# Kernel tuning notes

Measured on AMD Instinct MI355X. Metric: run time of the kernel, lower is better.

The kernel has to match this reference:

```python
import jax, jax.numpy as jnp
import numpy as np

B, N, D, H, DK, DV = 2, 2048, 1024, 16, 64, 64
NEG = -1000000000.0
EPS = 1e-6


def setup_inputs() -> dict:
    key = jax.random.key(0)
    ks = jax.random.split(key, 8)
    s = 0.02
    return {
        "q": jax.random.normal(ks[0], (B, N, D), jnp.float32),
        "k": jax.random.normal(ks[1], (B, N, D), jnp.float32),
        "v": jax.random.normal(ks[2], (B, N, D), jnp.float32),
        "attn_mask": jnp.ones((B, N, N), jnp.int32),
        "Wq": jax.random.normal(ks[3], (D, H * DK), jnp.float32) * s,
        "Wk": jax.random.normal(ks[4], (D, H * DK), jnp.float32) * s,
        "Wv": jax.random.normal(ks[5], (D, H * DV), jnp.float32) * s,
        "Wo": jax.random.normal(ks[6], (H * DV, D), jnp.float32) * s,
        "gamma": jnp.ones((D,), jnp.float32),
        "beta": jnp.zeros((D,), jnp.float32),
    }


def reference(q, k, v, attn_mask, Wq, Wk, Wv, Wo, gamma, beta):
    b, n, _ = q.shape
    residual = q
    # project and split heads: (b, h, n, dk)
    qh = (q @ Wq).reshape(b, n, H, DK).transpose(0, 2, 1, 3)
    kh = (k @ Wk).reshape(b, n, H, DK).transpose(0, 2, 1, 3)
    vh = (v @ Wv).reshape(b, n, H, DV).transpose(0, 2, 1, 3)
    temperature = DK ** 0.5
    scores = jnp.einsum('bhnd,bhmd->bhnm', qh / temperature, kh)
    # external mask (masked where mask == 0), broadcast over heads
    scores = jnp.where(attn_mask[:, None, :, :] == 0, NEG, scores)
    # built-in causal mask (strictly upper triangle)
    causal = jnp.triu(jnp.ones((n, n), dtype=bool), k=1)
    scores = jnp.where(causal, NEG, scores)
    attn = jax.nn.softmax(scores, axis=-1)
    out = jnp.einsum('bhnm,bhmd->bnhd', attn, vh).reshape(b, n, H * DV)
    out = out @ Wo + residual
    # LayerNorm(eps=1e-6)
    mean = out.mean(-1, keepdims=True)
    var = ((out - mean) ** 2).mean(-1, keepdims=True)
    out = (out - mean) / jnp.sqrt(var + EPS) * gamma + beta
    return out, attn
```

## Files before the change

### kernel.cpp

```cpp
#include <hip/hip_runtime.h>
#include <hip/hip_bf16.h>
#include <stdint.h>

#define B_ 2
#define N_ 2048
#define D_ 1024
#define H_ 16
#define MM 4096
#define NN 1024
#define KK 1024

typedef __bf16 bf16;
typedef __bf16 bf16x8 __attribute__((ext_vector_type(8)));
typedef float f32x4 __attribute__((ext_vector_type(4)));

struct __align__(8) bf4 { bf16 v[4]; };

#define LDS_STRIDE 144

#define GLDS(gp, lp)                                                     \
    __builtin_amdgcn_global_load_lds(                                    \
        (const __attribute__((address_space(1))) void*)(gp),             \
        (__attribute__((address_space(3))) void*)(lp), 16, 0, 0)

__global__ __launch_bounds__(256) void k_cvt3(const float* __restrict__ q,
                                              const float* __restrict__ k,
                                              const float* __restrict__ v,
                                              bf16* __restrict__ qb,
                                              bf16* __restrict__ kb,
                                              bf16* __restrict__ vb) {
    const int z = blockIdx.y;
    const float* s = z == 0 ? q : z == 1 ? k : v;
    bf16* d = z == 0 ? qb : z == 1 ? kb : vb;
    size_t i = ((size_t)blockIdx.x * 256 + threadIdx.x) * 8;
    f32x4 a = *(const f32x4*)(s + i);
    f32x4 b = *(const f32x4*)(s + i + 4);
    bf16x8 o;
#pragma unroll
    for (int j = 0; j < 4; ++j) { o[j] = (bf16)a[j]; o[4 + j] = (bf16)b[j]; }
    *(bf16x8*)(d + i) = o;
}

__global__ void k_wtt(const float* __restrict__ W, bf16* __restrict__ Wt) {
    __shared__ float t[32][33];
    int bx = blockIdx.x * 32, by = blockIdx.y * 32;
    int tx = threadIdx.x, ty = threadIdx.y;
#pragma unroll
    for (int j = 0; j < 32; j += 8)
        t[ty + j][tx] = W[(size_t)(by + ty + j) * 1024 + bx + tx];
    __syncthreads();
#pragma unroll
    for (int j = 0; j < 32; j += 8)
        Wt[(size_t)(bx + ty + j) * 1024 + by + tx] = (bf16)t[tx][ty + j];
}

__global__ __launch_bounds__(256) void k_bits(const int* __restrict__ mask,
                                              uint32_t* __restrict__ bits) {
    size_t flat = (size_t)blockIdx.x * 256 + threadIdx.x;
    int col = (int)(flat & (N_ - 1));
    int row = (int)((flat >> 11) & (N_ - 1));
    bool ok = (mask[flat] != 0) && (col <= row);
    unsigned long long bal = __ballot(ok);
    if ((threadIdx.x & 63) == 0)
        *(unsigned long long*)(bits + (flat >> 5)) = bal;
}

__device__ __forceinline__ void mm_core(const bf16* __restrict__ A,
                                        const bf16* __restrict__ Bt,
                                        int bm0, int bn0,
                                        bf16* As, bf16* Bs,
                                        f32x4 (&acc)[4][4]) {
    const int tid = threadIdx.x, w = tid >> 6, lane = tid & 63;
    const int g = lane >> 4, li = lane & 15;
    const int wr = w >> 1, wc = w & 1;
    const int row = tid >> 3, cc = tid & 7;

    f32x4 zz = {0.f, 0.f, 0.f, 0.f};
#pragma unroll
    for (int mf = 0; mf < 4; ++mf)
#pragma unroll
        for (int nf = 0; nf < 4; ++nf) acc[mf][nf] = zz;

    auto stage = [&](int k0) {
#pragma unroll
        for (int c = 0; c < 4; ++c) {
            int ch = c * 256 + tid;
            int r = ch >> 3, cl = ch & 7;
            GLDS(A + (size_t)(bm0 + r) * KK + k0 + cl * 8,
                 As + ((size_t)c * 256 + w * 64) * 8);
        }
#pragma unroll
        for (int c = 0; c < 4; ++c) {
            int ch = c * 256 + tid;
            int r = ch >> 3, cl = ch & 7;
            GLDS(Bt + (size_t)(bn0 + r) * KK + k0 + cl * 8,
                 Bs + ((size_t)c * 256 + w * 64) * 8);
        }
    };
    (void)row; (void)cc;

    stage(0);
    for (int s = 0; s < KK / 64; ++s) {
        __syncthreads();
#pragma unroll
        for (int kk = 0; kk < 2; ++kk) {
            bf16x8 af[4], bfr[4];
#pragma unroll
            for (int i = 0; i < 4; ++i) {
                af[i] = *(const bf16x8*)(As + (wr * 64 + i * 16 + li) * 64 + kk * 32 + g * 8);
                bfr[i] = *(const bf16x8*)(Bs + (wc * 64 + i * 16 + li) * 64 + kk * 32 + g * 8);
            }
#pragma unroll
            for (int mf = 0; mf < 4; ++mf)
#pragma unroll
                for (int nf = 0; nf < 4; ++nf)
                    acc[mf][nf] = __builtin_amdgcn_mfma_f32_16x16x32_bf16(
                        af[mf], bfr[nf], acc[mf][nf], 0, 0, 0);
        }
        __syncthreads();
        if (s + 1 < KK / 64) stage((s + 1) * 64);
    }
}

__global__ __launch_bounds__(256) void k_proj(const bf16* __restrict__ qb,
                                              const bf16* __restrict__ kb,
                                              const bf16* __restrict__ vb,
                                              const bf16* __restrict__ WqT,
                                              const bf16* __restrict__ WkT,
                                              const bf16* __restrict__ WvT,
                                              bf16* __restrict__ Qh,
                                              bf16* __restrict__ Kh,
                                              bf16* __restrict__ Vt) {
    __shared__ __align__(16) bf16 As[128 * 64];
    __shared__ __align__(16) bf16 Bs[128 * 64];
    const int z = blockIdx.y;
    const bf16* A = z == 0 ? qb : z == 1 ? kb : vb;
    const bf16* Bt = z == 0 ? WqT : z == 1 ? WkT : WvT;
    int bid = blockIdx.x;
    int swz = (bid & 7) * 32 + (bid >> 3);
    int bm0 = (swz >> 3) * 128, bn0 = (swz & 7) * 128;

    f32x4 acc[4][4];
    mm_core(A, Bt, bm0, bn0, As, Bs, acc);

    const int tid = threadIdx.x, w = tid >> 6, lane = tid & 63;
    const int g = lane >> 4, li = lane & 15;
    const int wr = w >> 1, wc = w & 1;
    const float scale = (z == 0) ? 0.125f : 1.0f;

    if (z < 2) {
        bf16* C = (z == 0) ? Qh : Kh;
#pragma unroll
        for (int mf = 0; mf < 4; ++mf)
#pragma unroll
            for (int nf = 0; nf < 4; ++nf) {
                int m0 = bm0 + wr * 64 + mf * 16 + g * 4;
                int n = bn0 + wc * 64 + nf * 16 + li;
#pragma unroll
                for (int r = 0; r < 4; ++r)
                    C[(size_t)(m0 + r) * NN + n] = (bf16)(acc[mf][nf][r] * scale);
            }
    } else {
#pragma unroll
        for (int mf = 0; mf < 4; ++mf)
#pragma unroll
            for (int nf = 0; nf < 4; ++nf) {
                int m0 = bm0 + wr * 64 + mf * 16 + g * 4;
                int n = bn0 + wc * 64 + nf * 16 + li;
                int bq = m0 >> 11, tok = m0 & (N_ - 1);
                int hh = n >> 6, dv = n & 63;
                bf4 val;
#pragma unroll
                for (int r = 0; r < 4; ++r) val.v[r] = (bf16)acc[mf][nf][r];
                *(bf4*)(Vt + ((size_t)((bq * H_ + hh) * 64 + dv)) * N_ + tok) = val;
            }
    }
}

__global__ __launch_bounds__(256) void k_out(const bf16* __restrict__ Ob,
                                             const bf16* __restrict__ WoT,
                                             float* __restrict__ outp,
                                             const float* __restrict__ resid) {
    __shared__ __align__(16) bf16 As[128 * 64];
    __shared__ __align__(16) bf16 Bs[128 * 64];
    int bid = blockIdx.x;
    int swz = (bid & 7) * 32 + (bid >> 3);
    int bm0 = (swz >> 3) * 128, bn0 = (swz & 7) * 128;

    f32x4 acc[4][4];
    mm_core(Ob, WoT, bm0, bn0, As, Bs, acc);

    const int tid = threadIdx.x, w = tid >> 6, lane = tid & 63;
    const int g = lane >> 4, li = lane & 15;
    const int wr = w >> 1, wc = w & 1;
#pragma unroll
    for (int mf = 0; mf < 4; ++mf)
#pragma unroll
        for (int nf = 0; nf < 4; ++nf) {
            int m0 = bm0 + wr * 64 + mf * 16 + g * 4;
            int n = bn0 + wc * 64 + nf * 16 + li;
#pragma unroll
            for (int r = 0; r < 4; ++r) {
                size_t ix = (size_t)(m0 + r) * NN + n;
                outp[ix] = acc[mf][nf][r] + resid[ix];
            }
        }
}

__global__ __launch_bounds__(256) void k_attn(const bf16* __restrict__ Qh,
                                              const bf16* __restrict__ Kh,
                                              const bf16* __restrict__ Vt,
                                              const uint32_t* __restrict__ bits,
                                              float* __restrict__ attnp,
                                              bf16* __restrict__ Ob) {
    __shared__ __align__(16) char Qs[64 * LDS_STRIDE];
    __shared__ __align__(16) char Ks[2][64 * LDS_STRIDE];
    __shared__ __align__(16) char Vs[2][64 * LDS_STRIDE];
    __shared__ __align__(16) char Ps[64 * LDS_STRIDE];
    const int tid = threadIdx.x, lane = tid & 63, w = tid >> 6;
    const int g = lane >> 4, li = lane & 15;
    const int p = blockIdx.x, h = blockIdx.y, b = blockIdx.z;
    const int srow = tid >> 3, sc = tid & 7;
    const int myrow = w * 16 + li;

    const size_t kbase = ((size_t)b * N_) * D_ + h * 64;
    const size_t vbase = ((size_t)(b * H_ + h) * 64) * N_;
    f32x4 zz = {0.f, 0.f, 0.f, 0.f};

    bf16x8 ka, kb2, va, vb2;
    auto loadK = [&](int jt) {
        const char* ks = (const char*)Kh +
            (kbase + (size_t)(jt * 64 + srow) * D_ + sc * 8) * 2;
        ka = *(const bf16x8*)ks;
        kb2 = *(const bf16x8*)(ks + (size_t)32 * D_ * 2);
    };
    auto loadV = [&](int jt) {
        const char* vs = (const char*)Vt +
            (vbase + (size_t)srow * N_ + jt * 64 + sc * 8) * 2;
        va = *(const bf16x8*)vs;
        vb2 = *(const bf16x8*)(vs + (size_t)32 * N_ * 2);
    };
    auto writeK = [&](int bi) {
        *(bf16x8*)(Ks[bi] + srow * LDS_STRIDE + sc * 16) = ka;
        *(bf16x8*)(Ks[bi] + (srow + 32) * LDS_STRIDE + sc * 16) = kb2;
    };
    auto writeV = [&](int bi) {
        *(bf16x8*)(Vs[bi] + srow * LDS_STRIDE + sc * 16) = va;
        *(bf16x8*)(Vs[bi] + (srow + 32) * LDS_STRIDE + sc * 16) = vb2;
    };

    for (int half = 0; half < 2; ++half) {
        const int qt = half ? (31 - p) : p;
        const int i0 = qt << 6;
        const size_t abase = (((size_t)b * H_ + h) * N_ + i0) * (size_t)N_;

        __syncthreads();
        {
            const char* qsrc = (const char*)Qh +
                (kbase + (size_t)(i0 + srow) * D_ + sc * 8) * 2;
            bf16x8 t0 = *(const bf16x8*)qsrc;
            bf16x8 t1 = *(const bf16x8*)(qsrc + (size_t)32 * D_ * 2);
            *(bf16x8*)(Qs + srow * LDS_STRIDE + sc * 16) = t0;
            *(bf16x8*)(Qs + (srow + 32) * LDS_STRIDE + sc * 16) = t1;
        }
        const uint32_t* mrow = bits + (((size_t)b * N_ + i0 + myrow) << 6);

        float m = -1e30f, l = 0.f;
        loadK(0);
        writeK(0);
        for (int jt = 0; jt <= qt; ++jt) {
            if (jt < qt) loadK(jt + 1);
            uint2 mw = *(const uint2*)(mrow + (jt << 1));
            __syncthreads();
            const char* Kb = Ks[jt & 1];

            f32x4 s[4];
#pragma unroll
            for (int mf = 0; mf < 4; ++mf) s[mf] = zz;
#pragma unroll
            for (int kk = 0; kk < 2; ++kk) {
                const int kb = kk * 64 + (g << 4);
                bf16x8 qf = *(const bf16x8*)(Qs + myrow * LDS_STRIDE + kb);
#pragma unroll
                for (int mf = 0; mf < 4; ++mf) {
                    bf16x8 kf = *(const bf16x8*)(Kb + (mf * 16 + li) * LDS_STRIDE + kb);
                    s[mf] = __builtin_amdgcn_mfma_f32_16x16x32_bf16(kf, qf, s[mf], 0, 0, 0);
                }
            }
            if (jt < qt) writeK((jt + 1) & 1);

            float tmax = m;
#pragma unroll
            for (int mf = 0; mf < 4; ++mf) {
                uint32_t wsel = (mf < 2) ? mw.x : mw.y;
#pragma unroll
                for (int r = 0; r < 4; ++r) {
                    int sh = (mf & 1) * 16 + g * 4 + r;
                    float xv = ((wsel >> sh) & 1) ? s[mf][r] : -1e9f;
                    s[mf][r] = xv;
                    tmax = fmaxf(tmax, xv);
                }
            }
            tmax = fmaxf(tmax, __shfl_xor(tmax, 16));
            tmax = fmaxf(tmax, __shfl_xor(tmax, 32));
            float ps = 0.f;
#pragma unroll
            for (int mf = 0; mf < 4; ++mf)
#pragma unroll
                for (int r = 0; r < 4; ++r) ps += __expf(s[mf][r] - tmax);
            ps += __shfl_xor(ps, 16);
            ps += __shfl_xor(ps, 32);
            l = l * __expf(m - tmax) + ps;
            m = tmax;
        }
        const float linv = 1.0f / l;

        f32x4 oacc[4];
#pragma unroll
        for (int nf = 0; nf < 4; ++nf) oacc[nf] = zz;

        __syncthreads();
        loadK(0);
        loadV(0);
        writeK(0);
        writeV(0);
        for (int jt = 0; jt <= qt; ++jt) {
            if (jt < qt) { loadK(jt + 1); loadV(jt + 1); }
            uint2 mw = *(const uint2*)(mrow + (jt << 1));
            __syncthreads();
            const char* Kb = Ks[jt & 1];
            const char* Vb = Vs[jt & 1];

            f32x4 s[4];
#pragma unroll
            for (int mf = 0; mf < 4; ++mf) s[mf] = zz;
#pragma unroll
            for (int kk = 0; kk < 2; ++kk) {
                const int kb = kk * 64 + (g << 4);
                bf16x8 qf = *(const bf16x8*)(Qs + myrow * LDS_STRIDE + kb);
#pragma unroll
                for (int mf = 0; mf < 4; ++mf) {
                    bf16x8 kf = *(const bf16x8*)(Kb + (mf * 16 + li) * LDS_STRIDE + kb);
                    s[mf] = __builtin_amdgcn_mfma_f32_16x16x32_bf16(kf, qf, s[mf], 0, 0, 0);
                }
            }
            if (jt < qt) { writeK((jt + 1) & 1); writeV((jt + 1) & 1); }

#pragma unroll
            for (int mf = 0; mf < 4; ++mf) {
                uint32_t wsel = (mf < 2) ? mw.x : mw.y;
#pragma unroll
                for (int r = 0; r < 4; ++r) {
                    int sh = (mf & 1) * 16 + g * 4 + r;
                    float xv = ((wsel >> sh) & 1) ? s[mf][r] : -1e9f;
                    s[mf][r] = __expf(xv - m) * linv;
                }
                __builtin_nontemporal_store(s[mf],
                    (f32x4*)(attnp + abase + (size_t)myrow * N_ + (jt << 6) + mf * 16 + g * 4));
                bf4 pk;
#pragma unroll
                for (int r = 0; r < 4; ++r) pk.v[r] = (bf16)s[mf][r];
                *(bf4*)(Ps + myrow * LDS_STRIDE + (mf * 16 + g * 4) * 2) = pk;
            }
#pragma unroll
            for (int kk = 0; kk < 2; ++kk) {
                const int kb = kk * 64 + (g << 4);
                bf16x8 pf = *(const bf16x8*)(Ps + myrow * LDS_STRIDE + kb);
#pragma unroll
                for (int nf = 0; nf < 4; ++nf) {
                    bf16x8 vf = *(const bf16x8*)(Vb + (nf * 16 + li) * LDS_STRIDE + kb);
                    oacc[nf] = __builtin_amdgcn_mfma_f32_16x16x32_bf16(pf, vf, oacc[nf], 0, 0, 0);
                }
            }
        }
#pragma unroll
        for (int nf = 0; nf < 4; ++nf)
#pragma unroll
            for (int r = 0; r < 4; ++r) {
                int gi = i0 + w * 16 + g * 4 + r;
                Ob[((size_t)(b * N_ + gi)) * D_ + h * 64 + nf * 16 + li] = (bf16)oacc[nf][r];
            }
        int zc0 = i0 + 64;
        if (zc0 < N_) {
            int r = tid >> 2, tc = tid & 3;
            f32x4 z = zz;
            for (int c = zc0 + tc * 4; c < N_; c += 16)
                __builtin_nontemporal_store(z, (f32x4*)(attnp + abase + (size_t)r * N_ + c));
        }
    }
}

__global__ __launch_bounds__(256) void k_ln(float* __restrict__ out,
                                            const float* __restrict__ gamma,
                                            const float* __restrict__ beta) {
    const int row = blockIdx.x, t = threadIdx.x, lane = t & 63, w = t >> 6;
    float* p = out + (size_t)row * D_;
    f32x4 x = *(const f32x4*)(p + t * 4);
    float s = x[0] + x[1] + x[2] + x[3];
    float s2 = x[0] * x[0] + x[1] * x[1] + x[2] * x[2] + x[3] * x[3];
#pragma unroll
    for (int o = 1; o < 64; o <<= 1) {
        s += __shfl_xor(s, o);
        s2 += __shfl_xor(s2, o);
    }
    __shared__ float r1[4], r2[4];
    if (lane == 0) { r1[w] = s; r2[w] = s2; }
    __syncthreads();
    s = r1[0] + r1[1] + r1[2] + r1[3];
    s2 = r2[0] + r2[1] + r2[2] + r2[3];
    float mean = s * (1.f / D_);
    float var = s2 * (1.f / D_) - mean * mean;
    float rstd = rsqrtf(var + 1e-6f);
    f32x4 gv = *(const f32x4*)(gamma + t * 4);
    f32x4 bv = *(const f32x4*)(beta + t * 4);
    f32x4 y;
#pragma unroll
    for (int c = 0; c < 4; ++c) y[c] = (x[c] - mean) * rstd * gv[c] + bv[c];
    *(f32x4*)(p + t * 4) = y;
}

extern "C" void kernel_launch(void* const* d_in, const int* in_sizes, int n_in,
                              void* d_out, int out_size, void* d_ws,
                              size_t ws_size, hipStream_t stream) {
    (void)in_sizes; (void)n_in; (void)out_size; (void)ws_size;
    const float* q = (const float*)d_in[0];
    const float* k = (const float*)d_in[1];
    const float* v = (const float*)d_in[2];
    const int* msk = (const int*)d_in[3];
    const float* Wq = (const float*)d_in[4];
    const float* Wk = (const float*)d_in[5];
    const float* Wv = (const float*)d_in[6];
    const float* Wo = (const float*)d_in[7];
    const float* gamma = (const float*)d_in[8];
    const float* beta = (const float*)d_in[9];

    float* outp = (float*)d_out;
    float* attnp = outp + (size_t)B_ * N_ * D_;

    const size_t U = (size_t)B_ * N_ * D_;
    const size_t W1 = (size_t)D_ * D_;
    bf16* ws = (bf16*)d_ws;
    bf16* qb = ws;   ws += U;
    bf16* kb = ws;   ws += U;
    bf16* vb = ws;   ws += U;
    bf16* WqT = ws;  ws += W1;
    bf16* WkT = ws;  ws += W1;
    bf16* WvT = ws;  ws += W1;
    bf16* WoT = ws;  ws += W1;
    bf16* Qh = ws;   ws += U;
    bf16* Kh = ws;   ws += U;
    bf16* Vt = ws;   ws += U;
    bf16* Ob = ws;   ws += U;
    uint32_t* bits = (uint32_t*)ws;

    k_cvt3<<<dim3(U / 8 / 256, 3), 256, 0, stream>>>(q, k, v, qb, kb, vb);
    dim3 tb(32, 8);
    k_wtt<<<dim3(32, 32), tb, 0, stream>>>(Wq, WqT);
    k_wtt<<<dim3(32, 32), tb, 0, stream>>>(Wk, WkT);
    k_wtt<<<dim3(32, 32), tb, 0, stream>>>(Wv, WvT);
    k_wtt<<<dim3(32, 32), tb, 0, stream>>>(Wo, WoT);
    k_bits<<<(size_t)B_ * N_ * N_ / 256, 256, 0, stream>>>(msk, bits);

    k_proj<<<dim3(256, 3), 256, 0, stream>>>(qb, kb, vb, WqT, WkT, WvT, Qh, Kh, Vt);

    k_attn<<<dim3(16, H_, B_), 256, 0, stream>>>(Qh, Kh, Vt, bits, attnp, Ob);

    k_out<<<256, 256, 0, stream>>>(Ob, WoT, outp, q);

    k_ln<<<B_ * N_, 256, 0, stream>>>(outp, gamma, beta);
}
```

Baseline: 300.2 us.

## Restructure attention into single-wave 16-row blocks with direct global K/V loads

Rewrites the attention kernel so each 64-thread block handles a 16-row query strip, paired with its mirrored strip for causal load balance. K and V fragments are read straight from global memory into registers instead of being staged through double-buffered LDS behind barriers. Blocks are mapped to (batch, head) so blocks sharing K/V land on the same XCD, for L2 reuse. The four weight-transpose launches are merged into one, trading launch overhead and more repeated global K/V reads for finer parallelism and no syncthreads.

```diff
diff --git a/kernel.cpp b/kernel.cpp
--- a/kernel.cpp
+++ b/kernel.cpp
@@ -41,7 +41,13 @@
     *(bf16x8*)(d + i) = o;
 }
 
-__global__ void k_wtt(const float* __restrict__ W, bf16* __restrict__ Wt) {
+__global__ void k_wtt4(const float* __restrict__ Wq, const float* __restrict__ Wk,
+                       const float* __restrict__ Wv, const float* __restrict__ Wo,
+                       bf16* __restrict__ WqT, bf16* __restrict__ WkT,
+                       bf16* __restrict__ WvT, bf16* __restrict__ WoT) {
+    const int z = blockIdx.z;
+    const float* W = z == 0 ? Wq : z == 1 ? Wk : z == 2 ? Wv : Wo;
+    bf16* Wt = z == 0 ? WqT : z == 1 ? WkT : z == 2 ? WvT : WoT;
     __shared__ float t[32][33];
     int bx = blockIdx.x * 32, by = blockIdx.y * 32;
     int tx = threadIdx.x, ty = threadIdx.y;
@@ -73,7 +79,6 @@
     const int tid = threadIdx.x, w = tid >> 6, lane = tid & 63;
     const int g = lane >> 4, li = lane & 15;
     const int wr = w >> 1, wc = w & 1;
-    const int row = tid >> 3, cc = tid & 7;
 
     f32x4 zz = {0.f, 0.f, 0.f, 0.f};
 #pragma unroll
@@ -97,7 +102,6 @@
                  Bs + ((size_t)c * 256 + w * 64) * 8);
         }
     };
-    (void)row; (void)cc;
 
     stage(0);
     for (int s = 0; s < KK / 64; ++s) {
@@ -207,88 +211,48 @@
         }
 }
 
-__global__ __launch_bounds__(256) void k_attn(const bf16* __restrict__ Qh,
-                                              const bf16* __restrict__ Kh,
-                                              const bf16* __restrict__ Vt,
-                                              const uint32_t* __restrict__ bits,
-                                              float* __restrict__ attnp,
-                                              bf16* __restrict__ Ob) {
-    __shared__ __align__(16) char Qs[64 * LDS_STRIDE];
-    __shared__ __align__(16) char Ks[2][64 * LDS_STRIDE];
-    __shared__ __align__(16) char Vs[2][64 * LDS_STRIDE];
-    __shared__ __align__(16) char Ps[64 * LDS_STRIDE];
-    const int tid = threadIdx.x, lane = tid & 63, w = tid >> 6;
+__global__ __launch_bounds__(64) void k_attn(const bf16* __restrict__ Qh,
+                                             const bf16* __restrict__ Kh,
+                                             const bf16* __restrict__ Vt,
+                                             const uint32_t* __restrict__ bits,
+                                             float* __restrict__ attnp,
+                                             bf16* __restrict__ Ob) {
+    __shared__ __align__(16) char Ps[16 * LDS_STRIDE];
+    const int lane = threadIdx.x;
     const int g = lane >> 4, li = lane & 15;
-    const int p = blockIdx.x, h = blockIdx.y, b = blockIdx.z;
-    const int srow = tid >> 3, sc = tid & 7;
-    const int myrow = w * 16 + li;
-
-    const size_t kbase = ((size_t)b * N_) * D_ + h * 64;
+    const int id = blockIdx.x;
+    const int xcd = id & 7, slot = id >> 3;
+    const int c = xcd + 8 * (slot & 3);
+    const int p = slot >> 2;
+    const int h = c >> 1, b = c & 1;
+
+    const size_t cbase = ((size_t)b * N_) * D_ + h * 64;
     const size_t vbase = ((size_t)(b * H_ + h) * 64) * N_;
-    f32x4 zz = {0.f, 0.f, 0.f, 0.f};
-
-    bf16x8 ka, kb2, va, vb2;
-    auto loadK = [&](int jt) {
-        const char* ks = (const char*)Kh +
-            (kbase + (size_t)(jt * 64 + srow) * D_ + sc * 8) * 2;
-        ka = *(const bf16x8*)ks;
-        kb2 = *(const bf16x8*)(ks + (size_t)32 * D_ * 2);
-    };
-    auto loadV = [&](int jt) {
-        const char* vs = (const char*)Vt +
-            (vbase + (size_t)srow * N_ + jt * 64 + sc * 8) * 2;
-        va = *(const bf16x8*)vs;
-        vb2 = *(const bf16x8*)(vs + (size_t)32 * N_ * 2);
-    };
-    auto writeK = [&](int bi) {
-        *(bf16x8*)(Ks[bi] + srow * LDS_STRIDE + sc * 16) = ka;
-        *(bf16x8*)(Ks[bi] + (srow + 32) * LDS_STRIDE + sc * 16) = kb2;
-    };
-    auto writeV = [&](int bi) {
-        *(bf16x8*)(Vs[bi] + srow * LDS_STRIDE + sc * 16) = va;
-        *(bf16x8*)(Vs[bi] + (srow + 32) * LDS_STRIDE + sc * 16) = vb2;
-    };
+    const f32x4 zz = {0.f, 0.f, 0.f, 0.f};
 
     for (int half = 0; half < 2; ++half) {
-        const int qt = half ? (31 - p) : p;
-        const int i0 = qt << 6;
-        const size_t abase = (((size_t)b * H_ + h) * N_ + i0) * (size_t)N_;
-
-        __syncthreads();
-        {
-            const char* qsrc = (const char*)Qh +
-                (kbase + (size_t)(i0 + srow) * D_ + sc * 8) * 2;
-            bf16x8 t0 = *(const bf16x8*)qsrc;
-            bf16x8 t1 = *(const bf16x8*)(qsrc + (size_t)32 * D_ * 2);
-            *(bf16x8*)(Qs + srow * LDS_STRIDE + sc * 16) = t0;
-            *(bf16x8*)(Qs + (srow + 32) * LDS_STRIDE + sc * 16) = t1;
-        }
-        const uint32_t* mrow = bits + (((size_t)b * N_ + i0 + myrow) << 6);
+        const int sl = half ? (127 - p) : p;
+        const int qs0 = sl << 4;
+        const int jt_max = sl >> 2;
+        const size_t abase = (((size_t)b * H_ + h) * N_ + qs0) * (size_t)N_;
+
+        const bf16* qptr = Qh + cbase + (size_t)(qs0 + li) * D_ + g * 8;
+        const bf16x8 qf0 = *(const bf16x8*)qptr;
+        const bf16x8 qf1 = *(const bf16x8*)(qptr + 32);
+        const uint32_t* mrow = bits + (((size_t)b * N_ + qs0 + li) << 6);
 
         float m = -1e30f, l = 0.f;
-        loadK(0);
-        writeK(0);
-        for (int jt = 0; jt <= qt; ++jt) {
-            if (jt < qt) loadK(jt + 1);
-            uint2 mw = *(const uint2*)(mrow + (jt << 1));
-            __syncthreads();
-            const char* Kb = Ks[jt & 1];
-
+        for (int jt = 0; jt <= jt_max; ++jt) {
+            const uint2 mw = *(const uint2*)(mrow + (jt << 1));
+            const bf16* kptr = Kh + cbase + (size_t)(jt * 64 + li) * D_ + g * 8;
             f32x4 s[4];
 #pragma unroll
-            for (int mf = 0; mf < 4; ++mf) s[mf] = zz;
-#pragma unroll
-            for (int kk = 0; kk < 2; ++kk) {
-                const int kb = kk * 64 + (g << 4);
-                bf16x8 qf = *(const bf16x8*)(Qs + myrow * LDS_STRIDE + kb);
-#pragma unroll
-                for (int mf = 0; mf < 4; ++mf) {
-                    bf16x8 kf = *(const bf16x8*)(Kb + (mf * 16 + li) * LDS_STRIDE + kb);
-                    s[mf] = __builtin_amdgcn_mfma_f32_16x16x32_bf16(kf, qf, s[mf], 0, 0, 0);
-                }
-            }
-            if (jt < qt) writeK((jt + 1) & 1);
-
+            for (int mf = 0; mf < 4; ++mf) {
+                bf16x8 k0 = *(const bf16x8*)(kptr + (size_t)(mf * 16) * D_);
+                bf16x8 k1 = *(const bf16x8*)(kptr + (size_t)(mf * 16) * D_ + 32);
+                s[mf] = __builtin_amdgcn_mfma_f32_16x16x32_bf16(k0, qf0, zz, 0, 0, 0);
+                s[mf] = __builtin_amdgcn_mfma_f32_16x16x32_bf16(k1, qf1, s[mf], 0, 0, 0);
+            }
             float tmax = m;
 #pragma unroll
             for (int mf = 0; mf < 4; ++mf) {
@@ -319,33 +283,17 @@
 #pragma unroll
         for (int nf = 0; nf < 4; ++nf) oacc[nf] = zz;
 
-        __syncthreads();
-        loadK(0);
-        loadV(0);
-        writeK(0);
-        writeV(0);
-        for (int jt = 0; jt <= qt; ++jt) {
-            if (jt < qt) { loadK(jt + 1); loadV(jt + 1); }
-            uint2 mw = *(const uint2*)(mrow + (jt << 1));
-            __syncthreads();
-            const char* Kb = Ks[jt & 1];
-            const char* Vb = Vs[jt & 1];
-
+        for (int jt = 0; jt <= jt_max; ++jt) {
+            const uint2 mw = *(const uint2*)(mrow + (jt << 1));
+            const bf16* kptr = Kh + cbase + (size_t)(jt * 64 + li) * D_ + g * 8;
             f32x4 s[4];
 #pragma unroll
-            for (int mf = 0; mf < 4; ++mf) s[mf] = zz;
-#pragma unroll
-            for (int kk = 0; kk < 2; ++kk) {
-                const int kb = kk * 64 + (g << 4);
-                bf16x8 qf = *(const bf16x8*)(Qs + myrow * LDS_STRIDE + kb);
-#pragma unroll
-                for (int mf = 0; mf < 4; ++mf) {
-                    bf16x8 kf = *(const bf16x8*)(Kb + (mf * 16 + li) * LDS_STRIDE + kb);
-                    s[mf] = __builtin_amdgcn_mfma_f32_16x16x32_bf16(kf, qf, s[mf], 0, 0, 0);
-                }
-            }
-            if (jt < qt) { writeK((jt + 1) & 1); writeV((jt + 1) & 1); }
-
+            for (int mf = 0; mf < 4; ++mf) {
+                bf16x8 k0 = *(const bf16x8*)(kptr + (size_t)(mf * 16) * D_);
+                bf16x8 k1 = *(const bf16x8*)(kptr + (size_t)(mf * 16) * D_ + 32);
+                s[mf] = __builtin_amdgcn_mfma_f32_16x16x32_bf16(k0, qf0, zz, 0, 0, 0);
+                s[mf] = __builtin_amdgcn_mfma_f32_16x16x32_bf16(k1, qf1, s[mf], 0, 0, 0);
+            }
 #pragma unroll
             for (int mf = 0; mf < 4; ++mf) {
                 uint32_t wsel = (mf < 2) ? mw.x : mw.y;
@@ -356,37 +304,34 @@
                     s[mf][r] = __expf(xv - m) * linv;
                 }
                 __builtin_nontemporal_store(s[mf],
-                    (f32x4*)(attnp + abase + (size_t)myrow * N_ + (jt << 6) + mf * 16 + g * 4));
+                    (f32x4*)(attnp + abase + (size_t)li * N_ + (jt << 6) + mf * 16 + g * 4));
                 bf4 pk;
 #pragma unroll
                 for (int r = 0; r < 4; ++r) pk.v[r] = (bf16)s[mf][r];
-                *(bf4*)(Ps + myrow * LDS_STRIDE + (mf * 16 + g * 4) * 2) = pk;
-            }
-#pragma unroll
-            for (int kk = 0; kk < 2; ++kk) {
-                const int kb = kk * 64 + (g << 4);
-                bf16x8 pf = *(const bf16x8*)(Ps + myrow * LDS_STRIDE + kb);
-#pragma unroll
-                for (int nf = 0; nf < 4; ++nf) {
-                    bf16x8 vf = *(const bf16x8*)(Vb + (nf * 16 + li) * LDS_STRIDE + kb);
-                    oacc[nf] = __builtin_amdgcn_mfma_f32_16x16x32_bf16(pf, vf, oacc[nf], 0, 0, 0);
-                }
+                *(bf4*)(Ps + li * LDS_STRIDE + (mf * 16 + g * 4) * 2) = pk;
+            }
+            bf16x8 pf0 = *(const bf16x8*)(Ps + li * LDS_STRIDE + g * 16);
+            bf16x8 pf1 = *(const bf16x8*)(Ps + li * LDS_STRIDE + 64 + g * 16);
+            const bf16* vp = Vt + vbase + (size_t)li * N_ + (jt << 6) + g * 8;
+#pragma unroll
+            for (int nf = 0; nf < 4; ++nf) {
+                bf16x8 v0 = *(const bf16x8*)(vp + (size_t)(nf * 16) * N_);
+                bf16x8 v1 = *(const bf16x8*)(vp + (size_t)(nf * 16) * N_ + 32);
+                oacc[nf] = __builtin_amdgcn_mfma_f32_16x16x32_bf16(pf0, v0, oacc[nf], 0, 0, 0);
+                oacc[nf] = __builtin_amdgcn_mfma_f32_16x16x32_bf16(pf1, v1, oacc[nf], 0, 0, 0);
             }
         }
 #pragma unroll
         for (int nf = 0; nf < 4; ++nf)
 #pragma unroll
             for (int r = 0; r < 4; ++r) {
-                int gi = i0 + w * 16 + g * 4 + r;
+                int gi = qs0 + g * 4 + r;
                 Ob[((size_t)(b * N_ + gi)) * D_ + h * 64 + nf * 16 + li] = (bf16)oacc[nf][r];
             }
-        int zc0 = i0 + 64;
-        if (zc0 < N_) {
-            int r = tid >> 2, tc = tid & 3;
-            f32x4 z = zz;
-            for (int c = zc0 + tc * 4; c < N_; c += 16)
-                __builtin_nontemporal_store(z, (f32x4*)(attnp + abase + (size_t)r * N_ + c));
-        }
+        const int z0 = (jt_max + 1) << 6;
+        float* arow = attnp + abase + (size_t)li * N_;
+        for (int c4 = (z0 >> 2) + g; c4 < N_ / 4; c4 += 4)
+            __builtin_nontemporal_store(zz, (f32x4*)(arow + c4 * 4));
     }
 }
 
@@ -454,16 +399,12 @@
     uint32_t* bits = (uint32_t*)ws;
 
     k_cvt3<<<dim3(U / 8 / 256, 3), 256, 0, stream>>>(q, k, v, qb, kb, vb);
-    dim3 tb(32, 8);
-    k_wtt<<<dim3(32, 32), tb, 0, stream>>>(Wq, WqT);
-    k_wtt<<<dim3(32, 32), tb, 0, stream>>>(Wk, WkT);
-    k_wtt<<<dim3(32, 32), tb, 0, stream>>>(Wv, WvT);
-    k_wtt<<<dim3(32, 32), tb, 0, stream>>>(Wo, WoT);
+    k_wtt4<<<dim3(32, 32, 4), dim3(32, 8), 0, stream>>>(Wq, Wk, Wv, Wo, WqT, WkT, WvT, WoT);
     k_bits<<<(size_t)B_ * N_ * N_ / 256, 256, 0, stream>>>(msk, bits);
 
     k_proj<<<dim3(256, 3), 256, 0, stream>>>(qb, kb, vb, WqT, WkT, WvT, Qh, Kh, Vt);
 
-    k_attn<<<dim3(16, H_, B_), 256, 0, stream>>>(Qh, Kh, Vt, bits, attnp, Ob);
+    k_attn<<<2048, 64, 0, stream>>>(Qh, Kh, Vt, bits, attnp, Ob);
 
     k_out<<<256, 256, 0, stream>>>(Ob, WoT, outp, q);
 
```

Result: slower. 341.2 us (+13.6%).
